# Performance work log

Hardware: AMD Instinct MI355X
Metric: run time of the kernel (lower is better)

The kernel has to match this reference:

```python
import jax, jax.numpy as jnp
import numpy as np

N_DOF = 7
HID = 128
BATCH = 65536
EPS_M = 1e-3      # mass-matrix PSD jitter
EPS_B = 1e-3      # friction-matrix PSD jitter
EPS_SOLVE = 1e-4  # jitter added before linalg.solve
N_CHOL = N_DOF * (N_DOF + 1) // 2  # 28
TRI_I, TRI_J = np.tril_indices(N_DOF)
DIAG_MASK = jnp.asarray(TRI_I == TRI_J)


def _mlp(x, p):
    # p = (W0,b0,W1,b1,W2,b2,W3,b3): Linear+Softplus x3 then Linear (n_layers=3)
    W0, b0, W1, b1, W2, b2, W3, b3 = p
    h = jax.nn.softplus(x @ W0 + b0)
    h = jax.nn.softplus(h @ W1 + b1)
    h = jax.nn.softplus(h @ W2 + b2)
    return h @ W3 + b3


def _psd(chol_vec, eps):
    # chol_vec: (n_chol,) lower-triangular entries row-major (i, j<=i); exp on diagonal
    vals = jnp.where(DIAG_MASK, jnp.exp(chol_vec), chol_vec)
    L = jnp.zeros((N_DOF, N_DOF), chol_vec.dtype).at[TRI_I, TRI_J].set(vals)
    return L @ L.T + eps * jnp.eye(N_DOF, dtype=chol_vec.dtype)


def _accel_single(q, qd, mp, pp, fp):
    mass = lambda qq: _psd(_mlp(qq, mp), EPS_M)

    def lagrangian(qq, qdd):
        M = mass(qq)
        V = jax.nn.softplus(_mlp(qq, pp))[0]
        return 0.5 * qdd @ (M @ qdd) - V

    dL_dq = jax.grad(lagrangian, argnums=0)(q, qd)
    # L is quadratic in qdot => Hessian wrt qdot (M_rows loop in torch) is exactly M(q)
    M = mass(q)
    # Coriolis_i = (d/dq [M(q) qd]_i) . qd  == jvp of q -> M(q) qd in direction qd
    _, coriolis = jax.jvp(lambda qq: mass(qq) @ qd, (q,), (qd,))
    B_mat = _psd(_mlp(q, fp), EPS_B)
    friction = B_mat @ qd
    rhs = dL_dq - coriolis - friction
    return jnp.linalg.solve(M + EPS_SOLVE * jnp.eye(N_DOF, dtype=q.dtype), rhs)


def setup_inputs() -> dict:
    key = jax.random.key(0)
    keys = iter(jax.random.split(key, 64))

    def lin(fan_in, fan_out):
        W = jax.random.normal(next(keys), (fan_in, fan_out), jnp.float32) / np.sqrt(fan_in)
        b = jax.random.normal(next(keys), (fan_out,), jnp.float32) * 0.01
        return W, b

    inp = {
        "q": jax.random.normal(next(keys), (BATCH, N_DOF), jnp.float32),
        "qdot": jax.random.normal(next(keys), (BATCH, N_DOF), jnp.float32),
    }
    for name, out_dim in [("m", N_CHOL), ("p", 1), ("f", N_CHOL)]:
        dims = [(N_DOF, HID), (HID, HID), (HID, HID), (HID, out_dim)]
        for li, (fi, fo) in enumerate(dims):
            W, b = lin(fi, fo)
            inp[f"{name}W{li}"] = W
            inp[f"{name}b{li}"] = b
    return inp


def reference(q, qdot,
              mW0, mb0, mW1, mb1, mW2, mb2, mW3, mb3,
              pW0, pb0, pW1, pb1, pW2, pb2, pW3, pb3,
              fW0, fb0, fW1, fb1, fW2, fb2, fW3, fb3):
    mp = (mW0, mb0, mW1, mb1, mW2, mb2, mW3, mb3)
    pp = (pW0, pb0, pW1, pb1, pW2, pb2, pW3, pb3)
    fp = (fW0, fb0, fW1, fb1, fW2, fb2, fW3, fb3)
    return jax.vmap(_accel_single, in_axes=(0, 0, None, None, None))(q, qdot, mp, pp, fp)
```

## Files before the change

### kernel.cpp

```cpp
#include <hip/hip_runtime.h>

#define NT 512
#define TM 32
#define NBLK (65536/TM)

typedef unsigned int u32;
typedef unsigned short u16;
typedef __attribute__((ext_vector_type(4))) float f32x4;
typedef __attribute__((ext_vector_type(8))) _Float16 f16x8;
typedef __attribute__((ext_vector_type(4))) _Float16 f16x4;

namespace {
constexpr int TI_[28] = {0,1,1,2,2,2,3,3,3,3,4,4,4,4,4,5,5,5,5,5,5,6,6,6,6,6,6,6};
constexpr int TJ_[28] = {0,0,1,0,1,2,0,1,2,3,0,1,2,3,4,0,1,2,3,4,5,0,1,2,3,4,5,6};
constexpr bool DG_[28] = {1,0,1,0,0,1,0,0,0,1,0,0,0,0,1,0,0,0,0,0,1,0,0,0,0,0,0,1};

constexpr int IB[20] = {0,16384,81920,147456,163840,180224,245760,311296,319488,
                        335872,401408,466944,475136,540672,606208,614400,630784,
                        696320,761856,778240};
constexpr int IN_[19]  = {128,128,128,32,128,128,128,16,128,128,128,16,128,128,16,128,128,128,32};
constexpr int ITY_[19] = {0,1,1,2,3,4,4,5,0,1,1,6,4,4,5,0,1,1,2};
constexpr int TOTF16 = 778240/2;
}

__device__ __forceinline__ float sp_f(float z) {
  float t = exp2f(-fabsf(z)*1.44269504f);
  return fmaxf(z, 0.f) + 0.69314718f*__log2f(1.f + t);
}
__device__ __forceinline__ float sigm_f(float z) {
  float t = exp2f(-z*1.44269504f);
  return __builtin_amdgcn_rcpf(1.f + t);
}
__device__ __forceinline__ float sig_a(float a) {
  return 1.f - exp2f(-a*1.44269504f);
}

__device__ __forceinline__ u16 h2b(_Float16 h) { union{_Float16 f; u16 u;} c; c.f = h; return c.u; }
__device__ __forceinline__ u16 f16b(float x)   { return h2b((_Float16)x); }
__device__ __forceinline__ float b2f(u16 b)    { union{u16 u; _Float16 f;} c; c.u = b; return (float)c.f; }
__device__ __forceinline__ f16x8 fz8()         { return (f16x8)(_Float16)0.f; }

__device__ __forceinline__ f32x4 mm(f16x8 a, f16x8 b, f32x4 c) {
  return __builtin_amdgcn_mfma_f32_16x16x32_f16(a, b, c, 0, 0, 0);
}

__device__ __forceinline__ f16x8 aread(const u16* P, int row, int s) {
  return *(const f16x8*)(P + row*128 + ((s ^ (row & 7)) << 3));
}
__device__ __forceinline__ int aidx4(int mrow, int n2) {
  return mrow*128 + (((n2 >> 3) ^ (mrow & 7)) << 3) + (n2 & 7);
}
__device__ __forceinline__ void awrite4(u16* P, int mrow, int n2, f16x4 v) {
  *(f16x4*)(P + aidx4(mrow, n2)) = v;
}
__device__ __forceinline__ f16x4 aread4(const u16* P, int mrow, int n2) {
  return *(const f16x4*)(P + aidx4(mrow, n2));
}
__device__ __forceinline__ f16x8 aq8(const u16* P, int row, int g) {
  f16x8 v = *(const f16x8*)(P + row*8);
  return g ? fz8() : v;
}
__device__ __forceinline__ f16x8 ubread(const u16* P, int row, int g) {
  return *(const f16x8*)(P + row*32 + ((g ^ (row & 3)) << 3));
}
__device__ __forceinline__ f16x8 bread(const char* img, int N, int sk, int n) {
  return *(const f16x8*)(img + ((sk*N + n) << 4));
}

struct __align__(16) Smem {
  u16 mh1[4096], mh2[4096], mh3[4096];
  u16 gA[4096], gB[4096];
  u16 pH1[4096], pH2[4096], pH3[4096];
  u16 qmh[256], qml[256], qdb[256];
  u16 ub[1024];
  float cTm[896];
  u16 dcH[896], cfH[896];
  float GQ1[384], GQp[384];
  float V[32];
};
static_assert(sizeof(Smem) <= 81920, "need 2 blocks/CU");

template<int KS, bool QSRC>
__device__ __forceinline__ void fwd_hl(const u16* Bh, const u16* Bl, u16* Oh, u16* Ol,
                                       const char* img, int hb, const float* bias,
                                       int wg, int l) {
  const int m = l & 15, g = l >> 4;
  f32x4 H[2][2], X[2][2];
  #pragma unroll
  for (int j=0;j<2;++j)
    #pragma unroll
    for (int mt=0;mt<2;++mt) { H[j][mt]=(f32x4){0,0,0,0}; X[j][mt]=(f32x4){0,0,0,0}; }
  #pragma unroll
  for (int ks=0; ks<KS; ++ks) {
    const int sk = ks*4 + g;
    f16x8 bh[2], bl[2];
    #pragma unroll
    for (int mt=0;mt<2;++mt) {
      const int row = mt*16+m;
      bh[mt] = QSRC ? aq8(Bh,row,g) : aread(Bh,row,sk);
      bl[mt] = QSRC ? aq8(Bl,row,g) : aread(Bl,row,sk);
    }
    #pragma unroll
    for (int j=0;j<2;++j) {
      const int n2t = wg + j*4;
      const f16x8 wh = bread(img,128,sk, n2t*16+m);
      const f16x8 wl = bread(img+hb,128,sk, n2t*16+m);
      #pragma unroll
      for (int mt=0;mt<2;++mt) {
        H[j][mt]=mm(wh,bh[mt],H[j][mt]);
        X[j][mt]=mm(wl,bh[mt],X[j][mt]);
        X[j][mt]=mm(wh,bl[mt],X[j][mt]);
      }
    }
  }
  #pragma unroll
  for (int j=0;j<2;++j) {
    const int n2 = (wg + j*4)*16 + 4*g;
    f32x4 bv = bias ? *(const f32x4*)(bias + n2) : (f32x4){0,0,0,0};
    #pragma unroll
    for (int mt=0;mt<2;++mt) {
      const int mrow = mt*16 + m;
      f16x4 vh, vl;
      #pragma unroll
      for (int r=0;r<4;++r) {
        const float o = sp_f(H[j][mt][r] + X[j][mt][r]*(1.f/4096.f) + bv[r]);
        const _Float16 hh = (_Float16)o;
        vh[r] = hh;
        vl[r] = (_Float16)((o - (float)hh)*4096.f);
      }
      awrite4(Oh, mrow, n2, vh);
      awrite4(Ol, mrow, n2, vl);
    }
  }
}

template<int KS, bool QSRC, int TC>
__device__ __forceinline__ void fwd_h(const u16* Bh, u16* Oh, const char* img,
                                      const float* bias, int tile0, int tstep, int l) {
  const int m = l & 15, g = l >> 4;
  f32x4 H[TC][2];
  #pragma unroll
  for (int j=0;j<TC;++j)
    #pragma unroll
    for (int mt=0;mt<2;++mt) H[j][mt]=(f32x4){0,0,0,0};
  #pragma unroll
  for (int ks=0; ks<KS; ++ks) {
    const int sk = ks*4 + g;
    f16x8 bh[2];
    #pragma unroll
    for (int mt=0;mt<2;++mt) {
      const int row = mt*16+m;
      bh[mt] = QSRC ? aq8(Bh,row,g) : aread(Bh,row,sk);
    }
    #pragma unroll
    for (int j=0;j<TC;++j) {
      const f16x8 wh = bread(img,128,sk,(tile0 + j*tstep)*16+m);
      #pragma unroll
      for (int mt=0;mt<2;++mt) H[j][mt]=mm(wh,bh[mt],H[j][mt]);
    }
  }
  #pragma unroll
  for (int j=0;j<TC;++j) {
    const int n2 = (tile0 + j*tstep)*16 + 4*g;
    f32x4 bv = bias ? *(const f32x4*)(bias + n2) : (f32x4){0,0,0,0};
    #pragma unroll
    for (int mt=0;mt<2;++mt) {
      const int mrow = mt*16 + m;
      f16x4 vh;
      #pragma unroll
      for (int r=0;r<4;++r) vh[r] = (_Float16)sp_f(H[j][mt][r] + bv[r]);
      awrite4(Oh, mrow, n2, vh);
    }
  }
}

__device__ __forceinline__ void grad128(const u16* Bin, const u16* Sig, u16* Out,
                                        const char* img, int wg, int l) {
  const int m = l & 15, g = l >> 4;
  f32x4 acc[2][2];
  #pragma unroll
  for (int j=0;j<2;++j)
    #pragma unroll
    for (int mt=0;mt<2;++mt) acc[j][mt]=(f32x4){0,0,0,0};
  #pragma unroll
  for (int ks=0; ks<4; ++ks) {
    const int sk = ks*4 + g;
    f16x8 bh[2];
    #pragma unroll
    for (int mt=0;mt<2;++mt) bh[mt] = aread(Bin, mt*16+m, sk);
    #pragma unroll
    for (int j=0;j<2;++j) {
      const f16x8 wh = bread(img,128,sk,(wg + j*4)*16+m);
      #pragma unroll
      for (int mt=0;mt<2;++mt) acc[j][mt]=mm(wh,bh[mt],acc[j][mt]);
    }
  }
  #pragma unroll
  for (int j=0;j<2;++j) {
    const int n2 = (wg + j*4)*16 + 4*g;
    #pragma unroll
    for (int mt=0;mt<2;++mt) {
      const int mrow = mt*16 + m;
      const f16x4 sg = aread4(Sig, mrow, n2);
      f16x4 o;
      #pragma unroll
      for (int r=0;r<4;++r) o[r] = (_Float16)(sig_a((float)sg[r]) * acc[j][mt][r]);
      awrite4(Out, mrow, n2, o);
    }
  }
}

template<int ASRC>
__device__ __forceinline__ void grad32(const u16* Bin, const u16* Sig, u16* Out,
                                       const char* img, int wg, int l) {
  const int m = l & 15, g = l >> 4;
  f32x4 acc[2][2];
  #pragma unroll
  for (int j=0;j<2;++j)
    #pragma unroll
    for (int mt=0;mt<2;++mt) acc[j][mt]=(f32x4){0,0,0,0};
  {
    f16x8 bh[2];
    #pragma unroll
    for (int mt=0;mt<2;++mt) {
      const int row = mt*16+m;
      bh[mt] = (ASRC==0) ? ubread(Bin,row,g) : aq8(Bin,row,g);
    }
    #pragma unroll
    for (int j=0;j<2;++j) {
      const f16x8 wh = bread(img,128,g,(wg + j*4)*16+m);
      #pragma unroll
      for (int mt=0;mt<2;++mt) acc[j][mt]=mm(wh,bh[mt],acc[j][mt]);
    }
  }
  #pragma unroll
  for (int j=0;j<2;++j) {
    const int n2 = (wg + j*4)*16 + 4*g;
    #pragma unroll
    for (int mt=0;mt<2;++mt) {
      const int mrow = mt*16 + m;
      const f16x4 sg = aread4(Sig, mrow, n2);
      f16x4 o;
      #pragma unroll
      for (int r=0;r<4;++r) o[r] = (_Float16)(sig_a((float)sg[r]) * acc[j][mt][r]);
      awrite4(Out, mrow, n2, o);
    }
  }
}

__device__ __forceinline__ void gradPotF(const u16* A3p, const float* V, float pb3v,
                                         const u16* Sig, u16* Out, const char* img,
                                         int wg, int l) {
  const int m = l & 15, g = l >> 4;
  float up[2];
  #pragma unroll
  for (int mt=0;mt<2;++mt) up[mt] = sigm_f(V[mt*16+m] + pb3v);
  f32x4 acc[2][2];
  #pragma unroll
  for (int j=0;j<2;++j)
    #pragma unroll
    for (int mt=0;mt<2;++mt) acc[j][mt]=(f32x4){0,0,0,0};
  #pragma unroll
  for (int ks=0; ks<4; ++ks) {
    const int sk = ks*4 + g;
    f16x8 bh[2];
    #pragma unroll
    for (int mt=0;mt<2;++mt) {
      const f16x8 a3 = aread(A3p, mt*16+m, sk);
      f16x8 t;
      #pragma unroll
      for (int e=0;e<8;++e) t[e] = (_Float16)(up[mt]*sig_a((float)a3[e]));
      bh[mt] = t;
    }
    #pragma unroll
    for (int j=0;j<2;++j) {
      const f16x8 wh = bread(img,128,sk,(wg + j*4)*16+m);
      #pragma unroll
      for (int mt=0;mt<2;++mt) acc[j][mt]=mm(wh,bh[mt],acc[j][mt]);
    }
  }
  #pragma unroll
  for (int j=0;j<2;++j) {
    const int n2 = (wg + j*4)*16 + 4*g;
    #pragma unroll
    for (int mt=0;mt<2;++mt) {
      const int mrow = mt*16 + m;
      const f16x4 sg = aread4(Sig, mrow, n2);
      f16x4 o;
      #pragma unroll
      for (int r=0;r<4;++r) o[r] = (_Float16)(sig_a((float)sg[r]) * acc[j][mt][r]);
      awrite4(Out, mrow, n2, o);
    }
  }
}

template<bool HL>
__device__ __forceinline__ void l3(const u16* Bh, const u16* Bl, const char* img, int hb,
                                   const float* b3, float* cT, u16* cH, int wg, int l) {
  const int m = l & 15, g = l >> 4;
  const int n2t = wg & 1, mt = wg >> 1;
  const int mrow = mt*16 + m;
  f32x4 H = {0,0,0,0}, X = {0,0,0,0};
  #pragma unroll
  for (int ks=0; ks<4; ++ks) {
    const int sk = ks*4 + g;
    const f16x8 bh = aread(Bh, mrow, sk);
    const f16x8 wh = bread(img,32,sk, n2t*16+m);
    H = mm(wh, bh, H);
    if (HL) {
      const f16x8 wl = bread(img+hb,32,sk, n2t*16+m);
      const f16x8 bl = aread(Bl, mrow, sk);
      X = mm(wl, bh, X);
      X = mm(wh, bl, X);
    }
  }
  const int u0 = n2t*16 + 4*g;
  if (u0 < 28) {
    f32x4 bv = b3 ? *(const f32x4*)(b3 + u0) : (f32x4){0,0,0,0};
    #pragma unroll
    for (int r=0;r<4;++r) {
      const float v = H[r] + (HL ? X[r]*(1.f/4096.f) : 0.f) + bv[r];
      if (HL) cT[(u0+r)*32 + mrow] = v;
      else    cH[(u0+r)*32 + mrow] = f16b(v);
    }
  }
}

template<bool HEAD>
__device__ __forceinline__ void n16(const u16* Bin, const char* img,
                                    float* GQ, float* V, int mt, int l) {
  const int m = l & 15, g = l >> 4;
  const int mrow = mt*16 + m;
  f32x4 acc = {0,0,0,0};
  #pragma unroll
  for (int ks=0; ks<4; ++ks) {
    const int sk = ks*4 + g;
    const f16x8 bh = aread(Bin, mrow, sk);
    const f16x8 wh = bread(img,16,sk,m);
    acc = mm(wh, bh, acc);
  }
  if (HEAD) {
    if (g == 0) V[mrow] = acc[0];
  } else {
    if (g < 2) {
      #pragma unroll
      for (int r=0;r<4;++r) GQ[mrow*12 + 4*g + r] = acc[r];
    }
  }
}

__global__ __launch_bounds__(256)
void pack_kernel(const float* __restrict__ mW0, const float* __restrict__ mb0,
                 const float* __restrict__ mW1, const float* __restrict__ mW2,
                 const float* __restrict__ mW3,
                 const float* __restrict__ pW0, const float* __restrict__ pb0,
                 const float* __restrict__ pW1, const float* __restrict__ pW2,
                 const float* __restrict__ pW3,
                 const float* __restrict__ fW0, const float* __restrict__ fb0,
                 const float* __restrict__ fW1, const float* __restrict__ fW2,
                 const float* __restrict__ fW3,
                 u16* __restrict__ ws)
{
  const int idx = blockIdx.x*256 + threadIdx.x;
  if (idx >= TOTF16) return;
  int img = 0;
  #pragma unroll
  for (int i = 1; i < 19; ++i) if (idx >= IB[i]/2) img = i;
  const int rem = idx - IB[img]/2;
  const int N = IN_[img];
  const int psz = (IB[img+1] - IB[img]) / 4;
  const int plane = rem >= psz;
  const int e = plane ? rem - psz : rem;
  const int slot = e / (N*8);
  const int r1 = e - slot*(N*8);
  const int n = r1 >> 3, ee = r1 & 7;
  const int k = slot*8 + ee;

  const float* W = nullptr; const float* B = nullptr;
  switch (img) {
    case 0:  W = mW0; B = mb0; break;
    case 1:  W = mW1; break;   case 2:  W = mW2; break;
    case 3:  W = mW3; break;   case 4:  W = mW3; break;
    case 5:  W = mW2; break;   case 6:  W = mW1; break;
    case 7:  W = mW0; break;
    case 8:  W = pW0; B = pb0; break;
    case 9:  W = pW1; break;   case 10: W = pW2; break;
    case 11: W = pW3; break;   case 12: W = pW2; break;
    case 13: W = pW1; break;   case 14: W = pW0; break;
    case 15: W = fW0; B = fb0; break;
    case 16: W = fW1; break;   case 17: W = fW2; break;
    default: W = fW3; break;
  }
  float v = 0.f;
  switch (ITY_[img]) {
    case 0: v = (k < 7) ? W[k*128 + n] : (k == 7 ? B[n] : 0.f); break;
    case 1: v = W[k*128 + n]; break;
    case 2: v = (n < 28) ? W[k*28 + n] : 0.f; break;
    case 3: v = (k < 28) ? W[n*28 + k] : 0.f; break;
    case 4: v = W[n*128 + k]; break;
    case 5: v = (n < 7) ? W[n*128 + k] : 0.f; break;
    default: v = (n == 0) ? W[k] : 0.f; break;
  }
  if (img == 12) v *= pW3[k];
  const _Float16 h = (_Float16)v;
  union { _Float16 f; u16 u; } c;
  c.f = plane ? (_Float16)((v - (float)h) * 4096.f) : h;
  ws[idx] = c.u;
}

__global__ __launch_bounds__(NT, 4)
void delan_kernel(const float* __restrict__ qg, const float* __restrict__ qdg,
    const float* __restrict__ mb1, const float* __restrict__ mb2, const float* __restrict__ mb3,
    const float* __restrict__ pb1, const float* __restrict__ pb2, const float* __restrict__ pb3,
    const float* __restrict__ fb1, const float* __restrict__ fb2, const float* __restrict__ fb3,
    const char* __restrict__ ws, float* __restrict__ out)
{
  __shared__ Smem S;
  const int t = threadIdx.x;
  const int l = t & 63;
  const int w = __builtin_amdgcn_readfirstlane(t >> 6);
  const int wg = w & 3;
  const int s0 = blockIdx.x * TM;

  if (t < 256) {
    const int m = t >> 3, c = t & 7;
    const float v = (c < 7) ? qg[(s0 + m)*7 + c] : 1.f;
    const _Float16 hh = (_Float16)v;
    S.qmh[t] = h2b(hh);
    S.qml[t] = f16b((v - (float)hh)*4096.f);
  } else {
    const int idx = t - 256;
    const int m = idx >> 3, c = idx & 7;
    S.qdb[idx] = (c < 7) ? f16b(qdg[(s0 + m)*7 + c]) : (u16)0;
  }
  __syncthreads();

  if (w < 4) fwd_hl<1,true>(S.qmh,S.qml,S.mh1,S.gA, ws+IB[0],(IB[1]-IB[0])/2, nullptr, wg, l);
  else       fwd_h<1,true,2>(S.qmh, S.pH1, ws+IB[8], nullptr, wg, 4, l);
  __syncthreads();
  if (w < 4) fwd_hl<4,false>(S.mh1,S.gA,S.mh2,S.gB, ws+IB[1],(IB[2]-IB[1])/2, mb1, wg, l);
  else       fwd_h<4,false,2>(S.pH1, S.pH2, ws+IB[9], pb1, wg, 4, l);
  __syncthreads();
  if (w < 4) fwd_hl<4,false>(S.mh2,S.gB,S.mh3,S.gA, ws+IB[2],(IB[3]-IB[2])/2, mb2, wg, l);
  else       fwd_h<4,false,2>(S.pH2, S.pH3, ws+IB[10], pb2, wg, 4, l);
  __syncthreads();
  if (w < 4)      l3<true>(S.mh3, S.gA, ws+IB[3],(IB[4]-IB[3])/2, mb3, S.cTm, nullptr, wg, l);
  else if (w < 6) n16<true>(S.pH3, ws+IB[11], nullptr, S.V, w-4, l);
  __syncthreads();
  if (w == 0 && l < 32) {
    const int ml = l;
    float qdv[7];
    #pragma unroll
    for (int i = 0; i < 7; ++i) qdv[i] = qdg[(s0 + ml)*7 + i];
    float vals[28], wvv[7] = {0,0,0,0,0,0,0};
    #pragma unroll
    for (int u = 0; u < 28; ++u) {
      const float cv = S.cTm[u*32 + ml];
      vals[u] = DG_[u] ? __expf(cv) : cv;
    }
    #pragma unroll
    for (int u = 0; u < 28; ++u) wvv[TJ_[u]] = fmaf(vals[u], qdv[TI_[u]], wvv[TJ_[u]]);
    #pragma unroll
    for (int u = 0; u < 28; ++u) S.cTm[u*32 + ml] = vals[u];
    #pragma unroll
    for (int u = 0; u < 28; ++u) {
      const float uval = (DG_[u] ? vals[u] : 1.f) * qdv[TI_[u]] * wvv[TJ_[u]];
      S.ub[ml*32 + (((u >> 3) ^ (ml & 3)) << 3) + (u & 7)] = f16b(uval);
    }
    #pragma unroll
    for (int u = 28; u < 32; ++u)
      S.ub[ml*32 + (((u >> 3) ^ (ml & 3)) << 3) + (u & 7)] = 0;
  } else if (w >= 4) {
    gradPotF(S.pH3, S.V, pb3[0], S.pH2, S.pH2, ws+IB[12], wg, l);
  }
  __syncthreads();
  if (w < 4) grad32<0>(S.ub, S.mh3, S.gB, ws+IB[4], wg, l);
  else       grad128(S.pH2, S.pH1, S.pH1, ws+IB[13], wg, l);
  __syncthreads();
  if (w < 4)      grad128(S.gB, S.mh2, S.gA, ws+IB[5], wg, l);
  else if (w < 6) n16<false>(S.pH1, ws+IB[14], S.GQp, nullptr, w-4, l);
  __syncthreads();
  if (w < 4) grad128(S.gA, S.mh1, S.gB, ws+IB[6], wg, l);
  else       grad32<1>(S.qdb, S.mh1, S.pH2, ws+IB[0], wg, l);
  __syncthreads();
  if (w < 2)      n16<false>(S.gB, ws+IB[7], S.GQ1, nullptr, w, l);
  else if (w < 4) fwd_h<1,true,4>(S.qmh, S.gA, ws+IB[15], nullptr, w-2, 2, l);
  else            grad128(S.pH2, S.mh2, S.pH3, ws+IB[1], wg, l);
  __syncthreads();
  if (w < 4) fwd_h<4,false,2>(S.gA, S.gB, ws+IB[16], fb1, wg, 4, l);
  else       grad128(S.pH3, S.mh3, S.pH2, ws+IB[2], wg, l);
  __syncthreads();
  if (w < 4) fwd_h<4,false,2>(S.gB, S.gA, ws+IB[17], fb2, wg, 4, l);
  else       l3<false>(S.pH2, nullptr, ws+IB[3], 0, nullptr, nullptr, S.dcH, wg, l);
  __syncthreads();
  if (w < 4) l3<false>(S.gA, nullptr, ws+IB[18], 0, fb3, nullptr, S.cfH, wg, l);
  __syncthreads();

  if (w == 0 && l < 32) {
    const int ml = l;
    float qdv[7];
    #pragma unroll
    for (int i = 0; i < 7; ++i) qdv[i] = qdg[(s0 + ml)*7 + i];
    float lv[28];
    #pragma unroll
    for (int u = 0; u < 28; ++u) lv[u] = S.cTm[u*32 + ml];
    float wvv[7] = {0,0,0,0,0,0,0};
    #pragma unroll
    for (int u = 0; u < 28; ++u) wvv[TJ_[u]] = fmaf(lv[u], qdv[TI_[u]], wvv[TJ_[u]]);
    float cor[7] = {0,0,0,0,0,0,0}, t2[7] = {0,0,0,0,0,0,0};
    #pragma unroll
    for (int u = 0; u < 28; ++u) {
      const float dv = (DG_[u] ? lv[u] : 1.f) * b2f(S.dcH[u*32 + ml]);
      cor[TI_[u]] = fmaf(dv, wvv[TJ_[u]], cor[TI_[u]]);
      t2[TJ_[u]]  = fmaf(dv, qdv[TI_[u]], t2[TJ_[u]]);
    }
    #pragma unroll
    for (int u = 0; u < 28; ++u) cor[TI_[u]] = fmaf(lv[u], t2[TJ_[u]], cor[TI_[u]]);
    float r7[7];
    #pragma unroll
    for (int i = 0; i < 7; ++i)
      r7[i] = S.GQ1[ml*12 + i] - cor[i] - S.GQp[ml*12 + i] - 1e-3f*qdv[i];
    float fv[28];
    #pragma unroll
    for (int u = 0; u < 28; ++u) {
      const float cv = b2f(S.cfH[u*32 + ml]);
      fv[u] = DG_[u] ? __expf(cv) : cv;
    }
    float wf[7] = {0,0,0,0,0,0,0};
    #pragma unroll
    for (int u = 0; u < 28; ++u) wf[TJ_[u]] = fmaf(fv[u], qdv[TI_[u]], wf[TJ_[u]]);
    #pragma unroll
    for (int u = 0; u < 28; ++u) r7[TI_[u]] -= fv[u]*wf[TJ_[u]];

    float L[7][7];
    #pragma unroll
    for (int i = 0; i < 7; ++i)
      #pragma unroll
      for (int j = 0; j < 7; ++j) L[i][j] = 0.f;
    #pragma unroll
    for (int u = 0; u < 28; ++u) L[TI_[u]][TJ_[u]] = lv[u];

    float M[7][7];
    #pragma unroll
    for (int i = 0; i < 7; ++i)
      #pragma unroll
      for (int j = 0; j < 7; ++j)
        if (j <= i) {
          float sum = (i == j) ? 1.1e-3f : 0.f;
          #pragma unroll
          for (int k = 0; k < 7; ++k) if (k <= j) sum = fmaf(L[i][k], L[j][k], sum);
          M[i][j] = sum;
        }
    float C[7][7];
    #pragma unroll
    for (int i = 0; i < 7; ++i)
      #pragma unroll
      for (int j = 0; j < 7; ++j)
        if (j <= i) {
          float sum = M[i][j];
          #pragma unroll
          for (int k = 0; k < 7; ++k) if (k < j) sum -= C[i][k] * C[j][k];
          if (j == i) C[i][j] = sqrtf(fmaxf(sum, 1e-12f));
          else        C[i][j] = sum / C[j][j];
        }
    float y[7];
    #pragma unroll
    for (int i = 0; i < 7; ++i) {
      float sum = r7[i];
      #pragma unroll
      for (int k = 0; k < 7; ++k) if (k < i) sum -= C[i][k] * y[k];
      y[i] = sum / C[i][i];
    }
    float x[7];
    #pragma unroll
    for (int i = 6; i >= 0; --i) {
      float sum = y[i];
      #pragma unroll
      for (int k = 0; k < 7; ++k) if (k > i) sum -= C[k][i] * x[k];
      x[i] = sum / C[i][i];
    }
    #pragma unroll
    for (int i = 0; i < 7; ++i) out[(s0 + ml)*7 + i] = x[i];
  }
}

extern "C" void kernel_launch(void* const* d_in, const int* in_sizes, int n_in,
                              void* d_out, int out_size, void* d_ws, size_t ws_size,
                              hipStream_t stream) {
  (void)in_sizes; (void)n_in; (void)out_size; (void)ws_size;
  const float* q   = (const float*)d_in[0];
  const float* qd  = (const float*)d_in[1];
  const float* mW0 = (const float*)d_in[2];  const float* mb0 = (const float*)d_in[3];
  const float* mW1 = (const float*)d_in[4];  const float* mb1 = (const float*)d_in[5];
  const float* mW2 = (const float*)d_in[6];  const float* mb2 = (const float*)d_in[7];
  const float* mW3 = (const float*)d_in[8];  const float* mb3 = (const float*)d_in[9];
  const float* pW0 = (const float*)d_in[10]; const float* pb0 = (const float*)d_in[11];
  const float* pW1 = (const float*)d_in[12]; const float* pb1 = (const float*)d_in[13];
  const float* pW2 = (const float*)d_in[14]; const float* pb2 = (const float*)d_in[15];
  const float* pW3 = (const float*)d_in[16]; const float* pb3 = (const float*)d_in[17];
  const float* fW0 = (const float*)d_in[18]; const float* fb0 = (const float*)d_in[19];
  const float* fW1 = (const float*)d_in[20]; const float* fb1 = (const float*)d_in[21];
  const float* fW2 = (const float*)d_in[22]; const float* fb2 = (const float*)d_in[23];
  const float* fW3 = (const float*)d_in[24]; const float* fb3 = (const float*)d_in[25];
  float* out = (float*)d_out;
  u16* ws = (u16*)d_ws;

  pack_kernel<<<dim3((TOTF16 + 255)/256), dim3(256), 0, stream>>>(
      mW0, mb0, mW1, mW2, mW3, pW0, pb0, pW1, pW2, pW3, fW0, fb0, fW1, fW2, fW3, ws);

  delan_kernel<<<dim3(NBLK), dim3(NT), 0, stream>>>(
      q, qd, mb1, mb2, mb3, pb1, pb2, pb3, fb1, fb2, fb3,
      (const char*)ws, out);
}
```

Measured before the change: 117.2 us.

## Reschedule MLP stages to shrink shared memory and fit three blocks per CU

Reorders the forward and backward MLP stages so the potential and friction networks run after the mass network and reuse its buffers. This cuts the shared-memory struct from eight 4096-entry activation buffers to five, and launch bounds rise to allow 3 blocks per CU. Some stages now split tiles across all 8 waves (TC=1) instead of 4 waves per network. The cost is more barrier-separated serial phases and less overlap between the independent networks, plus possible register pressure from the tighter launch bound.

```diff
diff --git a/kernel.cpp b/kernel.cpp
--- a/kernel.cpp
+++ b/kernel.cpp
@@ -69,25 +69,24 @@
 
 struct __align__(16) Smem {
   u16 mh1[4096], mh2[4096], mh3[4096];
-  u16 gA[4096], gB[4096];
-  u16 pH1[4096], pH2[4096], pH3[4096];
+  u16 X[4096], Y[4096];
   u16 qmh[256], qml[256], qdb[256];
   u16 ub[1024];
   float cTm[896];
   u16 dcH[896], cfH[896];
-  float GQ1[384], GQp[384];
+  float GQ1[256], GQp[256];
   float V[32];
 };
-static_assert(sizeof(Smem) <= 81920, "need 2 blocks/CU");
-
-template<int KS, bool QSRC>
+static_assert(sizeof(Smem) <= 54613, "need 3 blocks/CU");
+
+template<int KS, bool QSRC, int TC>
 __device__ __forceinline__ void fwd_hl(const u16* Bh, const u16* Bl, u16* Oh, u16* Ol,
                                        const char* img, int hb, const float* bias,
-                                       int wg, int l) {
+                                       int tile0, int tstep, int l) {
   const int m = l & 15, g = l >> 4;
-  f32x4 H[2][2], X[2][2];
-  #pragma unroll
-  for (int j=0;j<2;++j)
+  f32x4 H[TC][2], X[TC][2];
+  #pragma unroll
+  for (int j=0;j<TC;++j)
     #pragma unroll
     for (int mt=0;mt<2;++mt) { H[j][mt]=(f32x4){0,0,0,0}; X[j][mt]=(f32x4){0,0,0,0}; }
   #pragma unroll
@@ -101,10 +100,10 @@
       bl[mt] = QSRC ? aq8(Bl,row,g) : aread(Bl,row,sk);
     }
     #pragma unroll
-    for (int j=0;j<2;++j) {
-      const int n2t = wg + j*4;
-      const f16x8 wh = bread(img,128,sk, n2t*16+m);
-      const f16x8 wl = bread(img+hb,128,sk, n2t*16+m);
+    for (int j=0;j<TC;++j) {
+      const int n = (tile0 + j*tstep)*16 + m;
+      const f16x8 wh = bread(img,128,sk,n);
+      const f16x8 wl = bread(img+hb,128,sk,n);
       #pragma unroll
       for (int mt=0;mt<2;++mt) {
         H[j][mt]=mm(wh,bh[mt],H[j][mt]);
@@ -114,8 +113,8 @@
     }
   }
   #pragma unroll
-  for (int j=0;j<2;++j) {
-    const int n2 = (wg + j*4)*16 + 4*g;
+  for (int j=0;j<TC;++j) {
+    const int n2 = (tile0 + j*tstep)*16 + 4*g;
     f32x4 bv = bias ? *(const f32x4*)(bias + n2) : (f32x4){0,0,0,0};
     #pragma unroll
     for (int mt=0;mt<2;++mt) {
@@ -174,12 +173,13 @@
   }
 }
 
+template<int TC>
 __device__ __forceinline__ void grad128(const u16* Bin, const u16* Sig, u16* Out,
-                                        const char* img, int wg, int l) {
+                                        const char* img, int tile0, int tstep, int l) {
   const int m = l & 15, g = l >> 4;
-  f32x4 acc[2][2];
-  #pragma unroll
-  for (int j=0;j<2;++j)
+  f32x4 acc[TC][2];
+  #pragma unroll
+  for (int j=0;j<TC;++j)
     #pragma unroll
     for (int mt=0;mt<2;++mt) acc[j][mt]=(f32x4){0,0,0,0};
   #pragma unroll
@@ -189,15 +189,15 @@
     #pragma unroll
     for (int mt=0;mt<2;++mt) bh[mt] = aread(Bin, mt*16+m, sk);
     #pragma unroll
-    for (int j=0;j<2;++j) {
-      const f16x8 wh = bread(img,128,sk,(wg + j*4)*16+m);
+    for (int j=0;j<TC;++j) {
+      const f16x8 wh = bread(img,128,sk,(tile0 + j*tstep)*16+m);
       #pragma unroll
       for (int mt=0;mt<2;++mt) acc[j][mt]=mm(wh,bh[mt],acc[j][mt]);
     }
   }
   #pragma unroll
-  for (int j=0;j<2;++j) {
-    const int n2 = (wg + j*4)*16 + 4*g;
+  for (int j=0;j<TC;++j) {
+    const int n2 = (tile0 + j*tstep)*16 + 4*g;
     #pragma unroll
     for (int mt=0;mt<2;++mt) {
       const int mrow = mt*16 + m;
@@ -210,13 +210,13 @@
   }
 }
 
-template<int ASRC>
+template<int ASRC, int TC>
 __device__ __forceinline__ void grad32(const u16* Bin, const u16* Sig, u16* Out,
-                                       const char* img, int wg, int l) {
+                                       const char* img, int tile0, int tstep, int l) {
   const int m = l & 15, g = l >> 4;
-  f32x4 acc[2][2];
-  #pragma unroll
-  for (int j=0;j<2;++j)
+  f32x4 acc[TC][2];
+  #pragma unroll
+  for (int j=0;j<TC;++j)
     #pragma unroll
     for (int mt=0;mt<2;++mt) acc[j][mt]=(f32x4){0,0,0,0};
   {
@@ -227,15 +227,15 @@
       bh[mt] = (ASRC==0) ? ubread(Bin,row,g) : aq8(Bin,row,g);
     }
     #pragma unroll
-    for (int j=0;j<2;++j) {
-      const f16x8 wh = bread(img,128,g,(wg + j*4)*16+m);
+    for (int j=0;j<TC;++j) {
+      const f16x8 wh = bread(img,128,g,(tile0 + j*tstep)*16+m);
       #pragma unroll
       for (int mt=0;mt<2;++mt) acc[j][mt]=mm(wh,bh[mt],acc[j][mt]);
     }
   }
   #pragma unroll
-  for (int j=0;j<2;++j) {
-    const int n2 = (wg + j*4)*16 + 4*g;
+  for (int j=0;j<TC;++j) {
+    const int n2 = (tile0 + j*tstep)*16 + 4*g;
     #pragma unroll
     for (int mt=0;mt<2;++mt) {
       const int mrow = mt*16 + m;
@@ -248,16 +248,17 @@
   }
 }
 
+template<int TC>
 __device__ __forceinline__ void gradPotF(const u16* A3p, const float* V, float pb3v,
                                          const u16* Sig, u16* Out, const char* img,
-                                         int wg, int l) {
+                                         int tile0, int tstep, int l) {
   const int m = l & 15, g = l >> 4;
   float up[2];
   #pragma unroll
   for (int mt=0;mt<2;++mt) up[mt] = sigm_f(V[mt*16+m] + pb3v);
-  f32x4 acc[2][2];
-  #pragma unroll
-  for (int j=0;j<2;++j)
+  f32x4 acc[TC][2];
+  #pragma unroll
+  for (int j=0;j<TC;++j)
     #pragma unroll
     for (int mt=0;mt<2;++mt) acc[j][mt]=(f32x4){0,0,0,0};
   #pragma unroll
@@ -273,15 +274,15 @@
       bh[mt] = t;
     }
     #pragma unroll
-    for (int j=0;j<2;++j) {
-      const f16x8 wh = bread(img,128,sk,(wg + j*4)*16+m);
+    for (int j=0;j<TC;++j) {
+      const f16x8 wh = bread(img,128,sk,(tile0 + j*tstep)*16+m);
       #pragma unroll
       for (int mt=0;mt<2;++mt) acc[j][mt]=mm(wh,bh[mt],acc[j][mt]);
     }
   }
   #pragma unroll
-  for (int j=0;j<2;++j) {
-    const int n2 = (wg + j*4)*16 + 4*g;
+  for (int j=0;j<TC;++j) {
+    const int n2 = (tile0 + j*tstep)*16 + 4*g;
     #pragma unroll
     for (int mt=0;mt<2;++mt) {
       const int mrow = mt*16 + m;
@@ -344,7 +345,7 @@
   } else {
     if (g < 2) {
       #pragma unroll
-      for (int r=0;r<4;++r) GQ[mrow*12 + 4*g + r] = acc[r];
+      for (int r=0;r<4;++r) GQ[mrow*8 + 4*g + r] = acc[r];
     }
   }
 }
@@ -408,7 +409,7 @@
   ws[idx] = c.u;
 }
 
-__global__ __launch_bounds__(NT, 4)
+__global__ __launch_bounds__(NT, 6)
 void delan_kernel(const float* __restrict__ qg, const float* __restrict__ qdg,
     const float* __restrict__ mb1, const float* __restrict__ mb2, const float* __restrict__ mb3,
     const float* __restrict__ pb1, const float* __restrict__ pb2, const float* __restrict__ pb3,
@@ -435,17 +436,14 @@
   }
   __syncthreads();
 
-  if (w < 4) fwd_hl<1,true>(S.qmh,S.qml,S.mh1,S.gA, ws+IB[0],(IB[1]-IB[0])/2, nullptr, wg, l);
-  else       fwd_h<1,true,2>(S.qmh, S.pH1, ws+IB[8], nullptr, wg, 4, l);
-  __syncthreads();
-  if (w < 4) fwd_hl<4,false>(S.mh1,S.gA,S.mh2,S.gB, ws+IB[1],(IB[2]-IB[1])/2, mb1, wg, l);
-  else       fwd_h<4,false,2>(S.pH1, S.pH2, ws+IB[9], pb1, wg, 4, l);
-  __syncthreads();
-  if (w < 4) fwd_hl<4,false>(S.mh2,S.gB,S.mh3,S.gA, ws+IB[2],(IB[3]-IB[2])/2, mb2, wg, l);
-  else       fwd_h<4,false,2>(S.pH2, S.pH3, ws+IB[10], pb2, wg, 4, l);
-  __syncthreads();
-  if (w < 4)      l3<true>(S.mh3, S.gA, ws+IB[3],(IB[4]-IB[3])/2, mb3, S.cTm, nullptr, wg, l);
-  else if (w < 6) n16<true>(S.pH3, ws+IB[11], nullptr, S.V, w-4, l);
+  fwd_hl<1,true,1>(S.qmh, S.qml, S.mh1, S.X, ws+IB[0], (IB[1]-IB[0])/2, nullptr, w, 1, l);
+  __syncthreads();
+  fwd_hl<4,false,1>(S.mh1, S.X, S.mh2, S.Y, ws+IB[1], (IB[2]-IB[1])/2, mb1, w, 1, l);
+  __syncthreads();
+  fwd_hl<4,false,1>(S.mh2, S.Y, S.mh3, S.X, ws+IB[2], (IB[3]-IB[2])/2, mb2, w, 1, l);
+  __syncthreads();
+  if (w < 4) l3<true>(S.mh3, S.X, ws+IB[3], (IB[4]-IB[3])/2, mb3, S.cTm, nullptr, wg, l);
+  else       grad32<1,2>(S.qdb, S.mh1, S.Y, ws+IB[0], wg, 4, l);
   __syncthreads();
   if (w == 0 && l < 32) {
     const int ml = l;
@@ -471,29 +469,36 @@
     for (int u = 28; u < 32; ++u)
       S.ub[ml*32 + (((u >> 3) ^ (ml & 3)) << 3) + (u & 7)] = 0;
   } else if (w >= 4) {
-    gradPotF(S.pH3, S.V, pb3[0], S.pH2, S.pH2, ws+IB[12], wg, l);
-  }
-  __syncthreads();
-  if (w < 4) grad32<0>(S.ub, S.mh3, S.gB, ws+IB[4], wg, l);
-  else       grad128(S.pH2, S.pH1, S.pH1, ws+IB[13], wg, l);
-  __syncthreads();
-  if (w < 4)      grad128(S.gB, S.mh2, S.gA, ws+IB[5], wg, l);
-  else if (w < 6) n16<false>(S.pH1, ws+IB[14], S.GQp, nullptr, w-4, l);
-  __syncthreads();
-  if (w < 4) grad128(S.gA, S.mh1, S.gB, ws+IB[6], wg, l);
-  else       grad32<1>(S.qdb, S.mh1, S.pH2, ws+IB[0], wg, l);
-  __syncthreads();
-  if (w < 2)      n16<false>(S.gB, ws+IB[7], S.GQ1, nullptr, w, l);
-  else if (w < 4) fwd_h<1,true,4>(S.qmh, S.gA, ws+IB[15], nullptr, w-2, 2, l);
-  else            grad128(S.pH2, S.mh2, S.pH3, ws+IB[1], wg, l);
-  __syncthreads();
-  if (w < 4) fwd_h<4,false,2>(S.gA, S.gB, ws+IB[16], fb1, wg, 4, l);
-  else       grad128(S.pH3, S.mh3, S.pH2, ws+IB[2], wg, l);
-  __syncthreads();
-  if (w < 4) fwd_h<4,false,2>(S.gB, S.gA, ws+IB[17], fb2, wg, 4, l);
-  else       l3<false>(S.pH2, nullptr, ws+IB[3], 0, nullptr, nullptr, S.dcH, wg, l);
-  __syncthreads();
-  if (w < 4) l3<false>(S.gA, nullptr, ws+IB[18], 0, fb3, nullptr, S.cfH, wg, l);
+    grad128<2>(S.Y, S.mh2, S.X, ws+IB[1], wg, 4, l);
+  }
+  __syncthreads();
+  grad128<1>(S.X, S.mh3, S.Y, ws+IB[2], w, 1, l);
+  __syncthreads();
+  if (w < 4) l3<false>(S.Y, nullptr, ws+IB[3], 0, nullptr, nullptr, S.dcH, wg, l);
+  else       grad32<0,2>(S.ub, S.mh3, S.X, ws+IB[4], wg, 4, l);
+  __syncthreads();
+  grad128<1>(S.X, S.mh2, S.Y, ws+IB[5], w, 1, l);
+  __syncthreads();
+  grad128<1>(S.Y, S.mh1, S.X, ws+IB[6], w, 1, l);
+  __syncthreads();
+  if (w < 2)       n16<false>(S.X, ws+IB[7], S.GQ1, nullptr, w, l);
+  else if (w >= 4) fwd_h<1,true,2>(S.qmh, S.mh1, ws+IB[8], nullptr, wg, 4, l);
+  __syncthreads();
+  if (w < 4) fwd_h<4,false,2>(S.mh1, S.mh2, ws+IB[9], pb1, wg, 4, l);
+  else       fwd_h<1,true,2>(S.qmh, S.Y, ws+IB[15], nullptr, wg, 4, l);
+  __syncthreads();
+  if (w < 4) fwd_h<4,false,2>(S.mh2, S.mh3, ws+IB[10], pb2, wg, 4, l);
+  else       fwd_h<4,false,2>(S.Y, S.X, ws+IB[16], fb1, wg, 4, l);
+  __syncthreads();
+  if (w < 2)       n16<true>(S.mh3, ws+IB[11], nullptr, S.V, w, l);
+  else if (w >= 4) fwd_h<4,false,2>(S.X, S.Y, ws+IB[17], fb2, wg, 4, l);
+  __syncthreads();
+  if (w < 4) gradPotF<2>(S.mh3, S.V, pb3[0], S.mh2, S.mh2, ws+IB[12], wg, 4, l);
+  else       l3<false>(S.Y, nullptr, ws+IB[18], 0, fb3, nullptr, S.cfH, wg, l);
+  __syncthreads();
+  grad128<1>(S.mh2, S.mh1, S.X, ws+IB[13], w, 1, l);
+  __syncthreads();
+  if (w < 2) n16<false>(S.X, ws+IB[14], S.GQp, nullptr, w, l);
   __syncthreads();
 
   if (w == 0 && l < 32) {
@@ -519,7 +524,7 @@
     float r7[7];
     #pragma unroll
     for (int i = 0; i < 7; ++i)
-      r7[i] = S.GQ1[ml*12 + i] - cor[i] - S.GQp[ml*12 + i] - 1e-3f*qdv[i];
+      r7[i] = S.GQ1[ml*8 + i] - cor[i] - S.GQp[ml*8 + i] - 1e-3f*qdv[i];
     float fv[28];
     #pragma unroll
     for (int u = 0; u < 28; ++u) {
```

After: 123.7 us. 5.6% more time.
